# Performance work log

Measured on AMD Instinct MI355X. Metric: run time of the kernel, lower is better.

Reference implementation:

```python
import jax, jax.numpy as jnp
import numpy as np

B, S, D = 2, 2048, 1024
H = 16
HD = D // H  # 64


def setup_inputs() -> dict:
    key = jax.random.key(0)
    ks = jax.random.split(key, 6)
    sc = 1.0 / np.sqrt(D)
    x = jax.random.normal(ks[0], (B, S, D), dtype=jnp.float32)
    Wq = jax.random.normal(ks[1], (D, D), dtype=jnp.float32) * sc
    Wk = jax.random.normal(ks[2], (D, D), dtype=jnp.float32) * sc
    Wv = jax.random.normal(ks[3], (D, D), dtype=jnp.float32) * sc
    Wo = jax.random.normal(ks[4], (D, D), dtype=jnp.float32) * sc
    bo = jax.random.normal(ks[5], (D,), dtype=jnp.float32) * 0.01
    return {"x": x, "Wq": Wq, "Wk": Wk, "Wv": Wv, "Wo": Wo, "bo": bo}


def reference(x, Wq, Wk, Wv, Wo, bo):
    # projections: [B,S,D] -> [B,H,S,HD]
    def split_heads(t):
        return t.reshape(B, S, H, HD).transpose(0, 2, 1, 3)

    q = split_heads(x @ Wq)
    k = split_heads(x @ Wk)
    v = split_heads(x @ Wv)

    # naive full score matrix [B,H,S,S], masked causal, scaled softmax
    scores = jnp.einsum("bhqd,bhkd->bhqk", q, k)
    causal = jnp.tril(jnp.ones((S, S), dtype=bool))  # True = keep
    scores = jnp.where(causal, scores, -jnp.inf)
    attn = jax.nn.softmax(scores / np.sqrt(HD), axis=-1)

    ctx = jnp.einsum("bhqk,bhkd->bhqd", attn, v)  # [B,H,S,HD]
    ctx = ctx.transpose(0, 2, 1, 3).reshape(B, S, D)
    return ctx @ Wo + bo
```

## Files before the change

### kernel.cpp

```cpp
#include <hip/hip_runtime.h>

#define BB 2
#define SS 2048
#define DD 1024
#define HH 16
#define HD 64
#define MM (BB*SS)

typedef __bf16 bf16x8 __attribute__((ext_vector_type(8)));
typedef short  s16x4  __attribute__((ext_vector_type(4)));
typedef float  f32x4  __attribute__((ext_vector_type(4)));

#ifndef __has_builtin
#define __has_builtin(x) 0
#endif

__device__ __forceinline__ unsigned short f2bf(float f) {
    unsigned int u = __float_as_uint(f);
    u = (u + 0x7fffu + ((u >> 16) & 1u)) >> 16;
    return (unsigned short)u;
}
__device__ __forceinline__ unsigned int pack2(float a, float b) {
    return (unsigned int)f2bf(a) | ((unsigned int)f2bf(b) << 16);
}
__device__ __forceinline__ unsigned int pack2_fast(float a, float b) {
#if __has_builtin(__builtin_amdgcn_perm)
    return __builtin_amdgcn_perm(__float_as_uint(b) + 0x8000u,
                                 __float_as_uint(a) + 0x8000u, 0x07060302u);
#else
    return ((__float_as_uint(a) + 0x8000u) >> 16) |
           ((__float_as_uint(b) + 0x8000u) & 0xffff0000u);
#endif
}

__device__ __forceinline__ void gload_lds16(const unsigned short* g, unsigned short* l) {
    __builtin_amdgcn_global_load_lds(
        (const __attribute__((address_space(1))) void*)g,
        (__attribute__((address_space(3))) void*)l, 16, 0, 0);
}

__global__ __launch_bounds__(256) void prep_kernel(const float* __restrict__ x,
                                                   const float* __restrict__ Wq,
                                                   const float* __restrict__ Wk,
                                                   const float* __restrict__ Wv,
                                                   const float* __restrict__ Wo,
                                                   unsigned short* __restrict__ Xb,
                                                   unsigned short* __restrict__ Wqkvt,
                                                   unsigned short* __restrict__ Wot) {
    __shared__ float tile[32][33];
    const int bx = blockIdx.x;
    const int t = threadIdx.x;
    if (bx < 2048) {
        int gid = bx * 256 + t;
        int i = gid * 8;
        float4 a = *(const float4*)(x + i);
        float4 b = *(const float4*)(x + i + 4);
        uint4 o;
        o.x = pack2(a.x, a.y); o.y = pack2(a.z, a.w);
        o.z = pack2(b.x, b.y); o.w = pack2(b.z, b.w);
        ((uint4*)Xb)[gid] = o;
        return;
    }
    int pb = bx - 2048;
    int p = pb >> 10, rem = pb & 1023;
    int bxx = rem & 31, byy = rem >> 5;
    const float* src = (p == 0) ? Wq : (p == 1) ? Wk : (p == 2) ? Wv : Wo;
    unsigned short* dst = (p == 3) ? Wot : (Wqkvt + (size_t)p * DD * DD);
    int tx = t & 31, ty = t >> 5;
    int n = bxx * 32 + tx;
#pragma unroll
    for (int i = 0; i < 4; ++i) {
        int k = byy * 32 + ty + i * 8;
        tile[ty + i * 8][tx] = src[k * DD + n];
    }
    __syncthreads();
#pragma unroll
    for (int i = 0; i < 4; ++i) {
        int n2 = bxx * 32 + ty + i * 8;
        int k2 = byy * 32 + tx;
        dst[n2 * DD + k2] = f2bf(tile[tx][ty + i * 8]);
    }
}

#define GEMM_K_LOOP(Aglob, Bglob)                                                 \
    __shared__ unsigned short smem[128 * 132];                                    \
    unsigned short (*As)[64]  = (unsigned short(*)[64])smem;                      \
    unsigned short (*Bs)[64]  = (unsigned short(*)[64])(smem + 128 * 64);         \
    unsigned short (*Es)[132] = (unsigned short(*)[132])smem;                     \
    const int n0 = blockIdx.x * 128, m0 = blockIdx.y * 128;                       \
    const int t = threadIdx.x;                                                    \
    const int wave = t >> 6, lane = t & 63;                                       \
    const int wm = wave >> 1, wn = wave & 1;                                      \
    const int l15 = lane & 15, quad = lane >> 4;                                  \
    const int lr = lane >> 3, lg = (lane & 7);                                    \
    const int lc = (lg ^ lr) * 8;                    \
    f32x4 acc[4][4];                                                              \
    _Pragma("unroll") for (int i = 0; i < 4; ++i)                                 \
        _Pragma("unroll") for (int j = 0; j < 4; ++j) acc[i][j] = f32x4{0,0,0,0}; \
    for (int kt = 0; kt < 16; ++kt) {                                             \
        if (kt) __syncthreads();                                                  \
        _Pragma("unroll") for (int i = 0; i < 4; ++i) {                           \
            int row = wave * 32 + i * 8;                                          \
            gload_lds16(Aglob + (size_t)(m0 + row + lr) * DD + kt * 64 + lc, &As[row][0]); \
            gload_lds16(Bglob + (size_t)(n0 + row + lr) * DD + kt * 64 + lc, &Bs[row][0]); \
        }                                                                         \
        __syncthreads();                                                          \
        _Pragma("unroll") for (int kh = 0; kh < 2; ++kh) {                        \
            bf16x8 af[4], bfr[4];                                                 \
            _Pragma("unroll") for (int s = 0; s < 4; ++s)                         \
                af[s] = *(const bf16x8*)&As[wm * 64 + s * 16 + l15][((kh * 4 + quad) ^ (l15 & 7)) * 8]; \
            _Pragma("unroll") for (int s = 0; s < 4; ++s)                         \
                bfr[s] = *(const bf16x8*)&Bs[wn * 64 + s * 16 + l15][((kh * 4 + quad) ^ (l15 & 7)) * 8]; \
            _Pragma("unroll") for (int i = 0; i < 4; ++i)                         \
                _Pragma("unroll") for (int j = 0; j < 4; ++j)                     \
                    acc[i][j] = __builtin_amdgcn_mfma_f32_16x16x32_bf16(af[i], bfr[j], acc[i][j], 0, 0, 0); \
        }                                                                         \
    }                                                                             \
    __syncthreads();

__global__ __launch_bounds__(256) void qkv_gemm_kernel(const unsigned short* __restrict__ Xb,
                                                       const unsigned short* __restrict__ Wt,
                                                       unsigned short* __restrict__ Qg,
                                                       unsigned short* __restrict__ Kg,
                                                       unsigned short* __restrict__ Vt) {
    GEMM_K_LOOP(Xb, Wt)
    const int p = n0 >> 10;
    const float qs = (p == 0) ? 0.18033688011112042f : 1.0f;
    if (p < 2) {
#pragma unroll
        for (int sm = 0; sm < 4; ++sm)
#pragma unroll
            for (int sn = 0; sn < 4; ++sn)
#pragma unroll
                for (int i = 0; i < 4; ++i)
                    Es[wm * 64 + sm * 16 + quad * 4 + i][wn * 64 + sn * 16 + l15] = f2bf(acc[sm][sn][i] * qs);
    } else {
#pragma unroll
        for (int sm = 0; sm < 4; ++sm)
#pragma unroll
            for (int sn = 0; sn < 4; ++sn)
#pragma unroll
                for (int i = 0; i < 4; ++i)
                    Es[wn * 64 + sn * 16 + l15][wm * 64 + sm * 16 + quad * 4 + i] = f2bf(acc[sm][sn][i]);
    }
    __syncthreads();
    const int h0 = (n0 & 1023) >> 6;
    if (p < 2) {
        unsigned short* dst0 = p ? Kg : Qg;
        int ml = t >> 1, seg = t & 1;
        int gm = m0 + ml, b = gm >> 11, s = gm & 2047;
        unsigned short* dptr = dst0 + ((size_t)(b * HH + h0 + seg) * SS + s) * HD;
#pragma unroll
        for (int j = 0; j < 8; ++j)
            *(uint4*)(dptr + j * 8) = *(const uint4*)&Es[ml][seg * 64 + j * 8];
    } else {
        int nl = t >> 1, mh = t & 1;
        int h = h0 + (nl >> 6), hd = nl & 63;
        int b = m0 >> 11, s0 = (m0 & 2047) + mh * 64;
        unsigned short* dptr = Vt + ((size_t)(b * HH + h) * HD + hd) * SS + s0;
#pragma unroll
        for (int j = 0; j < 8; ++j)
            *(uint4*)(dptr + j * 8) = *(const uint4*)&Es[nl][mh * 64 + j * 8];
    }
}

__global__ __launch_bounds__(256) void out_gemm_kernel(const unsigned short* __restrict__ Ctxb,
                                                       const unsigned short* __restrict__ Wot,
                                                       const float* __restrict__ bo,
                                                       float* __restrict__ out) {
    GEMM_K_LOOP(Ctxb, Wot)
    (void)Es;
#pragma unroll
    for (int sn = 0; sn < 4; ++sn) {
        int gn = n0 + wn * 64 + sn * 16 + l15;
        float bias = bo[gn];
#pragma unroll
        for (int sm = 0; sm < 4; ++sm)
#pragma unroll
            for (int i = 0; i < 4; ++i) {
                int gm = m0 + wm * 64 + sm * 16 + quad * 4 + i;
                out[(size_t)gm * DD + gn] = acc[sm][sn][i] + bias;
            }
    }
}

__global__ __launch_bounds__(256) void attn_kernel(const unsigned short* __restrict__ Qg,
                                                   const unsigned short* __restrict__ Kg,
                                                   const unsigned short* __restrict__ Vt,
                                                   unsigned short* __restrict__ Ctxb) {
    __shared__ unsigned short Ks[2][128][64];
    __shared__ unsigned short Vs[2][64][128];

    const int bh = blockIdx.x;
    const int qt = (int)gridDim.y - 1 - (int)blockIdx.y;
    const int t = threadIdx.x;
    const int wave = t >> 6, lane = t & 63;
    const int l15 = lane & 15, quad = lane >> 4;
    const int q0 = qt * 128;
    const int b = bh >> 4, h = bh & 15;

    const unsigned short* Qb = Qg + (size_t)bh * SS * HD;
    const unsigned short* Kb = Kg + (size_t)bh * SS * HD;
    const unsigned short* Vb = Vt + (size_t)bh * HD * SS;

    int qrow[2];
    bf16x8 bq[2][2];
#pragma unroll
    for (int u = 0; u < 2; ++u) {
        qrow[u] = q0 + wave * 32 + u * 16 + l15;
#pragma unroll
        for (int hh = 0; hh < 2; ++hh)
            bq[u][hh] = *(const bf16x8*)(Qb + (size_t)qrow[u] * HD + hh * 32 + quad * 8);
    }

    const int rloc = lane >> 3, pcl = lane & 7;
    const int vrl = lane >> 4, vgc = lane & 15;
    const unsigned short* ksrc[4];
    const unsigned short* vsrc[4];
#pragma unroll
    for (int j = 0; j < 4; ++j) {
        int krow = (wave * 4 + j) * 8 + rloc;
        ksrc[j] = Kb + (size_t)krow * HD + (pcl ^ rloc) * 8;
        int vrow = wave * 16 + j * 4 + vrl;
        vsrc[j] = Vb + (size_t)vrow * SS + (vgc ^ (vrow & 15)) * 8;
    }

    f32x4 acc[2][4];
#pragma unroll
    for (int u = 0; u < 2; ++u)
#pragma unroll
        for (int db = 0; db < 4; ++db) acc[u][db] = f32x4{0, 0, 0, 0};
    float lsum[2] = {0.f, 0.f};
    const int nkt = qt + 1;
    const int kbtail = wave * 2 + 2;

#pragma unroll
    for (int j = 0; j < 4; ++j) {
        gload_lds16(ksrc[j], &Ks[0][(wave * 4 + j) * 8][0]);
        gload_lds16(vsrc[j], &Vs[0][wave * 16 + j * 4][0]);
    }
    __syncthreads();

    for (int kt = 0; kt < nkt; ++kt) {
        const int buf = kt & 1;
        const int k0 = kt * 128;
        if (kt + 1 < nkt) {
            const int nb = buf ^ 1;
#pragma unroll
            for (int j = 0; j < 4; ++j) {
                gload_lds16(ksrc[j] + (size_t)(kt + 1) * 128 * HD, &Ks[nb][(wave * 4 + j) * 8][0]);
                gload_lds16(vsrc[j] + (kt + 1) * 128,              &Vs[nb][wave * 16 + j * 4][0]);
            }
        }

        auto tile_body = [&](int kbmax, bool tail) {
#pragma unroll
            for (int kb = 0; kb < 8; ++kb) {
                if (kb >= kbmax) continue;
                bf16x8 ak[2];
#pragma unroll
                for (int hh = 0; hh < 2; ++hh)
                    ak[hh] = *(const bf16x8*)&Ks[buf][kb * 16 + l15][((hh * 4 + quad) ^ (l15 & 7)) * 8];
                f32x4 St[2] = {f32x4{0, 0, 0, 0}, f32x4{0, 0, 0, 0}};
                __builtin_amdgcn_s_setprio(1);
#pragma unroll
                for (int u = 0; u < 2; ++u)
#pragma unroll
                    for (int hh = 0; hh < 2; ++hh)
                        St[u] = __builtin_amdgcn_mfma_f32_16x16x32_bf16(ak[hh], bq[u][hh], St[u], 0, 0, 0);
                __builtin_amdgcn_s_setprio(0);
                s16x4 ap[2];
#pragma unroll
                for (int u = 0; u < 2; ++u) {
                    if (tail) {
#pragma unroll
                        for (int r = 0; r < 4; ++r)
                            if (k0 + kb * 16 + quad * 4 + r > qrow[u]) St[u][r] = -1e30f;
                    }
                    float e0 = __builtin_amdgcn_exp2f(St[u][0]);
                    float e1 = __builtin_amdgcn_exp2f(St[u][1]);
                    float e2 = __builtin_amdgcn_exp2f(St[u][2]);
                    float e3 = __builtin_amdgcn_exp2f(St[u][3]);
                    lsum[u] += (e0 + e1) + (e2 + e3);
                    uint2 uu;
                    uu.x = pack2_fast(e0, e1);
                    uu.y = pack2_fast(e2, e3);
                    ap[u] = *(s16x4*)&uu;
                }
                __builtin_amdgcn_s_setprio(1);
#pragma unroll
                for (int db = 0; db < 4; ++db) {
                    const int pg = (2 * kb + (quad >> 1)) ^ l15;
                    s16x4 bv = *(const s16x4*)&Vs[buf][db * 16 + l15][pg * 8 + (quad & 1) * 4];
#pragma unroll
                    for (int u = 0; u < 2; ++u)
                        acc[u][db] = __builtin_amdgcn_mfma_f32_16x16x16bf16_1k(ap[u], bv, acc[u][db], 0, 0, 0);
                }
                __builtin_amdgcn_s_setprio(0);
            }
        };
        if (kt == nkt - 1) tile_body(kbtail, true);
        else               tile_body(8, false);

        __syncthreads();
    }

#pragma unroll
    for (int u = 0; u < 2; ++u) {
        float lu = lsum[u];
        lu += __shfl_xor(lu, 16, 64);
        lu += __shfl_xor(lu, 32, 64);
        float linv = 1.0f / lu;
#pragma unroll
        for (int r = 0; r < 4; ++r) {
            float ir = __shfl(linv, quad * 4 + r, 64);
            int gq = q0 + wave * 32 + u * 16 + quad * 4 + r;
            size_t base = ((size_t)(b * SS + gq)) * DD + h * HD;
#pragma unroll
            for (int db = 0; db < 4; ++db)
                Ctxb[base + db * 16 + l15] = f2bf(acc[u][db][r] * ir);
        }
    }
}

extern "C" void kernel_launch(void* const* d_in, const int* in_sizes, int n_in,
                              void* d_out, int out_size, void* d_ws, size_t ws_size,
                              hipStream_t stream) {
    const float* x  = (const float*)d_in[0];
    const float* Wq = (const float*)d_in[1];
    const float* Wk = (const float*)d_in[2];
    const float* Wv = (const float*)d_in[3];
    const float* Wo = (const float*)d_in[4];
    const float* bo = (const float*)d_in[5];
    float* out = (float*)d_out;

    char* w = (char*)d_ws;
    unsigned short* Xb    = (unsigned short*)(w);
    unsigned short* Wqkvt = (unsigned short*)(w + (size_t)(8 << 20));
    unsigned short* Wot   = (unsigned short*)(w + (size_t)(14 << 20));
    unsigned short* Qg    = (unsigned short*)(w + (size_t)(16 << 20));
    unsigned short* Kg    = (unsigned short*)(w + (size_t)(24 << 20));
    unsigned short* Vt    = (unsigned short*)(w + (size_t)(32 << 20));
    unsigned short* Ctxb  = (unsigned short*)(w + (size_t)(40 << 20));

    prep_kernel<<<6144, 256, 0, stream>>>(x, Wq, Wk, Wv, Wo, Xb, Wqkvt, Wot);
    qkv_gemm_kernel<<<dim3(3 * DD / 128, MM / 128), 256, 0, stream>>>(Xb, Wqkvt, Qg, Kg, Vt);
    attn_kernel<<<dim3(BB * HH, SS / 128), 256, 0, stream>>>(Qg, Kg, Vt, Ctxb);
    out_gemm_kernel<<<dim3(DD / 128, MM / 128), 256, 0, stream>>>(Ctxb, Wot, bo, out);
}
```

Before: 186.4 us.

## Pair short and long causal query tiles per block and pre-swizzle V layout

Each attention block now handles two 64-row query tiles, one near the start and one near the end of the sequence, so every block does roughly the same causal work. Both tiles share the same K/V tile loads from LDS. The V^T store in the QKV GEMM epilogue now writes a pre-swizzled layout, which lets the attention kernel load V linearly and read it with a simpler XOR index. This trades extra branching per kb step, plus a dependency on a matched layout between two kernels, for even load balance and less tail imbalance.

```diff
diff --git a/kernel.cpp b/kernel.cpp
--- a/kernel.cpp
+++ b/kernel.cpp
@@ -156,11 +156,16 @@
     } else {
         int nl = t >> 1, mh = t & 1;
         int h = h0 + (nl >> 6), hd = nl & 63;
-        int b = m0 >> 11, s0 = (m0 & 2047) + mh * 64;
-        unsigned short* dptr = Vt + ((size_t)(b * HH + h) * HD + hd) * SS + s0;
-#pragma unroll
-        for (int j = 0; j < 8; ++j)
-            *(uint4*)(dptr + j * 8) = *(const uint4*)&Es[nl][mh * 64 + j * 8];
+        int b = m0 >> 11;
+        const int o = hd & 15, e = o & ~1, sw = o & 1;
+        unsigned short* rowp = Vt + ((size_t)(b * HH + h) * HD + hd) * SS + (m0 & 2047);
+#pragma unroll
+        for (int j = 0; j < 8; ++j) {
+            uint4 v = *(const uint4*)&Es[nl][mh * 64 + j * 8];
+            if (sw) { unsigned t0 = v.x, t1 = v.y; v.x = v.z; v.y = v.w; v.z = t0; v.w = t1; }
+            int Q = (mh * 16 + 2 * j) ^ e;
+            *(uint4*)(rowp + Q * 4) = v;
+        }
     }
 }
 
@@ -192,11 +197,14 @@
     __shared__ unsigned short Vs[2][64][128];
 
     const int bh = blockIdx.x;
-    const int qt = (int)gridDim.y - 1 - (int)blockIdx.y;
+    const int pr = blockIdx.y;
+    const int qtA = pr, qtB = 31 - pr;
+    const int nktA = (qtA >> 1) + 1;
+    const int nktB = (qtB >> 1) + 1;
     const int t = threadIdx.x;
     const int wave = t >> 6, lane = t & 63;
     const int l15 = lane & 15, quad = lane >> 4;
-    const int q0 = qt * 128;
+    const int q0A = qtA * 64, q0B = qtB * 64;
     const int b = bh >> 4, h = bh & 15;
 
     const unsigned short* Qb = Qg + (size_t)bh * SS * HD;
@@ -204,14 +212,14 @@
     const unsigned short* Vb = Vt + (size_t)bh * HD * SS;
 
     int qrow[2];
+    qrow[0] = q0A + wave * 16 + l15;
+    qrow[1] = q0B + wave * 16 + l15;
     bf16x8 bq[2][2];
 #pragma unroll
-    for (int u = 0; u < 2; ++u) {
-        qrow[u] = q0 + wave * 32 + u * 16 + l15;
+    for (int u = 0; u < 2; ++u)
 #pragma unroll
         for (int hh = 0; hh < 2; ++hh)
             bq[u][hh] = *(const bf16x8*)(Qb + (size_t)qrow[u] * HD + hh * 32 + quad * 8);
-    }
 
     const int rloc = lane >> 3, pcl = lane & 7;
     const int vrl = lane >> 4, vgc = lane & 15;
@@ -222,7 +230,7 @@
         int krow = (wave * 4 + j) * 8 + rloc;
         ksrc[j] = Kb + (size_t)krow * HD + (pcl ^ rloc) * 8;
         int vrow = wave * 16 + j * 4 + vrl;
-        vsrc[j] = Vb + (size_t)vrow * SS + (vgc ^ (vrow & 15)) * 8;
+        vsrc[j] = Vb + (size_t)vrow * SS + vgc * 8;
     }
 
     f32x4 acc[2][4];
@@ -231,8 +239,6 @@
 #pragma unroll
         for (int db = 0; db < 4; ++db) acc[u][db] = f32x4{0, 0, 0, 0};
     float lsum[2] = {0.f, 0.f};
-    const int nkt = qt + 1;
-    const int kbtail = wave * 2 + 2;
 
 #pragma unroll
     for (int j = 0; j < 4; ++j) {
@@ -241,10 +247,10 @@
     }
     __syncthreads();
 
-    for (int kt = 0; kt < nkt; ++kt) {
+    for (int kt = 0; kt < nktB; ++kt) {
         const int buf = kt & 1;
         const int k0 = kt * 128;
-        if (kt + 1 < nkt) {
+        if (kt + 1 < nktB) {
             const int nb = buf ^ 1;
 #pragma unroll
             for (int j = 0; j < 4; ++j) {
@@ -253,56 +259,69 @@
             }
         }
 
-        auto tile_body = [&](int kbmax, bool tail) {
-#pragma unroll
-            for (int kb = 0; kb < 8; ++kb) {
-                if (kb >= kbmax) continue;
-                bf16x8 ak[2];
+        const bool tail0 = (kt == nktA - 1), tail1 = (kt == nktB - 1);
+        const int kbmax0 = (kt < nktA) ? (tail0 ? ((q0A - k0) >> 4) + wave + 1 : 8) : 0;
+        const int kbmax1 = tail1 ? ((q0B - k0) >> 4) + wave + 1 : 8;
+
+#pragma unroll
+        for (int kb = 0; kb < 8; ++kb) {
+            if (kb >= kbmax1) continue;
+            const bool do0 = kb < kbmax0;
+            bf16x8 ak[2];
+#pragma unroll
+            for (int hh = 0; hh < 2; ++hh)
+                ak[hh] = *(const bf16x8*)&Ks[buf][kb * 16 + l15][((hh * 4 + quad) ^ (l15 & 7)) * 8];
+            f32x4 St1 = f32x4{0, 0, 0, 0};
+#pragma unroll
+            for (int hh = 0; hh < 2; ++hh)
+                St1 = __builtin_amdgcn_mfma_f32_16x16x32_bf16(ak[hh], bq[1][hh], St1, 0, 0, 0);
+            f32x4 St0 = f32x4{0, 0, 0, 0};
+            if (do0) {
 #pragma unroll
                 for (int hh = 0; hh < 2; ++hh)
-                    ak[hh] = *(const bf16x8*)&Ks[buf][kb * 16 + l15][((hh * 4 + quad) ^ (l15 & 7)) * 8];
-                f32x4 St[2] = {f32x4{0, 0, 0, 0}, f32x4{0, 0, 0, 0}};
-                __builtin_amdgcn_s_setprio(1);
-#pragma unroll
-                for (int u = 0; u < 2; ++u)
-#pragma unroll
-                    for (int hh = 0; hh < 2; ++hh)
-                        St[u] = __builtin_amdgcn_mfma_f32_16x16x32_bf16(ak[hh], bq[u][hh], St[u], 0, 0, 0);
-                __builtin_amdgcn_s_setprio(0);
-                s16x4 ap[2];
-#pragma unroll
-                for (int u = 0; u < 2; ++u) {
-                    if (tail) {
-#pragma unroll
-                        for (int r = 0; r < 4; ++r)
-                            if (k0 + kb * 16 + quad * 4 + r > qrow[u]) St[u][r] = -1e30f;
-                    }
-                    float e0 = __builtin_amdgcn_exp2f(St[u][0]);
-                    float e1 = __builtin_amdgcn_exp2f(St[u][1]);
-                    float e2 = __builtin_amdgcn_exp2f(St[u][2]);
-                    float e3 = __builtin_amdgcn_exp2f(St[u][3]);
-                    lsum[u] += (e0 + e1) + (e2 + e3);
-                    uint2 uu;
-                    uu.x = pack2_fast(e0, e1);
-                    uu.y = pack2_fast(e2, e3);
-                    ap[u] = *(s16x4*)&uu;
-                }
-                __builtin_amdgcn_s_setprio(1);
-#pragma unroll
-                for (int db = 0; db < 4; ++db) {
-                    const int pg = (2 * kb + (quad >> 1)) ^ l15;
-                    s16x4 bv = *(const s16x4*)&Vs[buf][db * 16 + l15][pg * 8 + (quad & 1) * 4];
-#pragma unroll
-                    for (int u = 0; u < 2; ++u)
-                        acc[u][db] = __builtin_amdgcn_mfma_f32_16x16x16bf16_1k(ap[u], bv, acc[u][db], 0, 0, 0);
-                }
-                __builtin_amdgcn_s_setprio(0);
-            }
-        };
-        if (kt == nkt - 1) tile_body(kbtail, true);
-        else               tile_body(8, false);
-
-        __syncthreads();
+                    St0 = __builtin_amdgcn_mfma_f32_16x16x32_bf16(ak[hh], bq[0][hh], St0, 0, 0, 0);
+            }
+            if (tail1) {
+#pragma unroll
+                for (int r = 0; r < 4; ++r)
+                    if (k0 + kb * 16 + quad * 4 + r > qrow[1]) St1[r] = -1e30f;
+            }
+            if (do0 && tail0) {
+#pragma unroll
+                for (int r = 0; r < 4; ++r)
+                    if (k0 + kb * 16 + quad * 4 + r > qrow[0]) St0[r] = -1e30f;
+            }
+            float e0 = __builtin_amdgcn_exp2f(St1[0]);
+            float e1 = __builtin_amdgcn_exp2f(St1[1]);
+            float e2 = __builtin_amdgcn_exp2f(St1[2]);
+            float e3 = __builtin_amdgcn_exp2f(St1[3]);
+            lsum[1] += (e0 + e1) + (e2 + e3);
+            uint2 uu1;
+            uu1.x = pack2_fast(e0, e1);
+            uu1.y = pack2_fast(e2, e3);
+            s16x4 ap1 = *(s16x4*)&uu1;
+            s16x4 ap0;
+            if (do0) {
+                float f0 = __builtin_amdgcn_exp2f(St0[0]);
+                float f1 = __builtin_amdgcn_exp2f(St0[1]);
+                float f2 = __builtin_amdgcn_exp2f(St0[2]);
+                float f3 = __builtin_amdgcn_exp2f(St0[3]);
+                lsum[0] += (f0 + f1) + (f2 + f3);
+                uint2 uu0;
+                uu0.x = pack2_fast(f0, f1);
+                uu0.y = pack2_fast(f2, f3);
+                ap0 = *(s16x4*)&uu0;
+            }
+#pragma unroll
+            for (int db = 0; db < 4; ++db) {
+                s16x4 bv = *(const s16x4*)&Vs[buf][db * 16 + l15][((4 * kb + quad) ^ l15) * 4];
+                acc[1][db] = __builtin_amdgcn_mfma_f32_16x16x16bf16_1k(ap1, bv, acc[1][db], 0, 0, 0);
+                if (do0)
+                    acc[0][db] = __builtin_amdgcn_mfma_f32_16x16x16bf16_1k(ap0, bv, acc[0][db], 0, 0, 0);
+            }
+        }
+
+        if (kt + 1 < nktB) __syncthreads();
     }
 
 #pragma unroll
@@ -311,10 +330,11 @@
         lu += __shfl_xor(lu, 16, 64);
         lu += __shfl_xor(lu, 32, 64);
         float linv = 1.0f / lu;
+        const int q0u = u ? q0B : q0A;
 #pragma unroll
         for (int r = 0; r < 4; ++r) {
             float ir = __shfl(linv, quad * 4 + r, 64);
-            int gq = q0 + wave * 32 + u * 16 + quad * 4 + r;
+            int gq = q0u + wave * 16 + quad * 4 + r;
             size_t base = ((size_t)(b * SS + gq)) * DD + h * HD;
 #pragma unroll
             for (int db = 0; db < 4; ++db)
@@ -345,6 +365,6 @@
 
     prep_kernel<<<6144, 256, 0, stream>>>(x, Wq, Wk, Wv, Wo, Xb, Wqkvt, Wot);
     qkv_gemm_kernel<<<dim3(3 * DD / 128, MM / 128), 256, 0, stream>>>(Xb, Wqkvt, Qg, Kg, Vt);
-    attn_kernel<<<dim3(BB * HH, SS / 128), 256, 0, stream>>>(Qg, Kg, Vt, Ctxb);
+    attn_kernel<<<dim3(BB * HH, 16), 256, 0, stream>>>(Qg, Kg, Vt, Ctxb);
     out_gemm_kernel<<<dim3(DD / 128, MM / 128), 256, 0, stream>>>(Ctxb, Wot, bo, out);
 }
```

Measured after the change: 194.2 us. 1.04x slower.
